# Performance work log

Measured on AMD Instinct MI355X. Metric: run time of the kernel, lower is better.

## Reference

```python
import jax, jax.numpy as jnp
import numpy as np

V, D, H, M, E, K = 32000, 1024, 1024, 64, 8, 2
B, S = 2, 2048


def _w(k, shape):
    fan_in = shape[-2] if len(shape) > 1 else shape[-1]
    return (jax.random.normal(k, shape, jnp.float32) / np.sqrt(fan_in)).astype(jnp.float32)


def setup_inputs() -> dict:
    key = jax.random.key(0)
    ks = jax.random.split(key, 24)
    HE = H // 2  # expert hidden = 512
    return {
        "input_ids": jax.random.randint(ks[0], (B, S), 0, V, dtype=jnp.int64),
        "emb": _w(ks[1], (V, D)),
        "enc_W": _w(ks[2], (D, H)), "enc_b": jnp.zeros((H,), jnp.float32),
        "s2c_W": _w(ks[3], (H, M)), "s2c_b": jnp.zeros((M,), jnp.float32),
        "rW1": _w(ks[4], (M, 64)), "rb1": jnp.zeros((64,), jnp.float32),
        "rW2": _w(ks[5], (64, E)), "rb2": jnp.zeros((E,), jnp.float32),
        "eW1": _w(ks[6], (E, M, HE)), "eb1": jnp.zeros((E, HE), jnp.float32),
        "eW2": _w(ks[7], (E, HE, M)), "eb2": jnp.zeros((E, M), jnp.float32),
        "c2s_W": _w(ks[8], (M, H)), "c2s_b": jnp.zeros((H,), jnp.float32),
        "dec_W": _w(ks[9], (H, D)), "dec_b": jnp.zeros((D,), jnp.float32),
        "out_W": _w(ks[10], (D, V)), "out_b": jnp.zeros((V,), jnp.float32),
    }


def reference(input_ids, emb, enc_W, enc_b, s2c_W, s2c_b, rW1, rb1, rW2, rb2,
              eW1, eb1, eW2, eb2, c2s_W, c2s_b, dec_W, dec_b, out_W, out_b):
    b, s = input_ids.shape
    n = b * s
    num_e = rW2.shape[1]
    # 1) embed + GIF encoder (linear + sigmoid spike-rate surrogate)
    x = emb[input_ids]                                   # (B,S,D)
    spikes_enc = jax.nn.sigmoid(x @ enc_W + enc_b)       # (B,S,H)
    # 2) spike -> continuous (rate coding over time window, then linear)
    cont = spikes_enc.reshape(n, -1) @ s2c_W + s2c_b     # (N,M)
    # 3) liquid MoE router: tanh MLP gate, softmax, top-k, renormalize
    gate_h = jnp.tanh(cont @ rW1 + rb1)
    probs = jax.nn.softmax(gate_h @ rW2 + rb2, axis=-1)  # (N,E)
    topv, topi = jax.lax.top_k(probs, K)                 # (N,K)
    wts = topv / jnp.sum(topv, axis=-1, keepdims=True)
    # per-token dense combine weights (zero for unselected experts) — matches
    # the original mask-and-sum over the full expert loop
    w_full = jnp.zeros((n, num_e), cont.dtype).at[jnp.arange(n)[:, None], topi].add(wts)
    # 4) all experts on all tokens (as in the source loop), then weighted combine
    h1 = jax.nn.relu(jnp.einsum('nm,emh->enh', cont, eW1) + eb1[:, None, :])  # (E,N,H/2)
    eo = jnp.einsum('enh,ehm->enm', h1, eW2) + eb2[:, None, :]                # (E,N,M)
    expert_out = jnp.einsum('ne,enm->nm', w_full, eo)                         # (N,M)
    # 5) continuous -> spike (Poisson expected rate) then time-average
    spikes_moe = jax.nn.sigmoid(expert_out @ c2s_W + c2s_b)                   # (N,H)
    spikes_avg = spikes_moe.reshape(b, s, -1)                                 # (B,S,H)
    # 6) GIF decoder + output projection
    decoded = jax.nn.sigmoid(spikes_avg @ dec_W + dec_b)                      # (B,S,D)
    logits = decoded @ out_W + out_b                                          # (B,S,V)
    return (logits, probs.reshape(b, s, num_e))
```

## Files before the change

kernel.cpp:

```cpp
#include <hip/hip_runtime.h>
#include <hip/hip_bf16.h>
#include <math.h>


typedef __bf16 bf16x8 __attribute__((ext_vector_type(8)));
typedef float f32x4 __attribute__((ext_vector_type(4)));

__device__ __forceinline__ ushort f2bf(float f) {
  union { float f; unsigned u; } v; v.f = f;
  unsigned u = v.u;
  u += 0x7FFFu + ((u >> 16) & 1u);
  return (ushort)(u >> 16);
}

__device__ __forceinline__ void async16(const void* g, void* l) {
  __builtin_amdgcn_global_load_lds((const __attribute__((address_space(1))) void*)g,
                                   (__attribute__((address_space(3))) void*)l,
                                   16, 0, 0);
}

__global__ void pack_w_kernel(const float* __restrict__ W, ushort* __restrict__ Wpk,
                              int K, int N) {
  long t = (long)blockIdx.x * blockDim.x + threadIdx.x;
  long total = (long)(K >> 3) * N;
  if (t >= total) return;
  long kb = t / N;
  int n = (int)(t - kb * N);
  long zoff = (long)blockIdx.y * K * N;
  const float* src = W + zoff + (kb * 8) * (long)N + n;
  union { ushort u[8]; uint4 v; } o;
#pragma unroll
  for (int j = 0; j < 8; ++j) o.u[j] = f2bf(src[(long)j * N]);
  *(uint4*)(Wpk + zoff + t * 8) = o.v;
}

__global__ void embed_pk_kernel(const int* __restrict__ ids, const float* __restrict__ emb,
                                ushort* __restrict__ xpk, int M) {
  int m = blockIdx.x * blockDim.x + threadIdx.x;
  int kb = blockIdx.y;
  long id = ids[m];
  const float4* s = (const float4*)(emb + id * 1024 + kb * 8);
  float4 a = s[0], b = s[1];
  union { ushort u[8]; uint4 v; } o;
  o.u[0] = f2bf(a.x); o.u[1] = f2bf(a.y); o.u[2] = f2bf(a.z); o.u[3] = f2bf(a.w);
  o.u[4] = f2bf(b.x); o.u[5] = f2bf(b.y); o.u[6] = f2bf(b.z); o.u[7] = f2bf(b.w);
  *(uint4*)(xpk + ((size_t)kb * M + m) * 8) = o.v;
}

template <int WAVES_M, int WAVES_N, int WM, int WN, int ACT, int OUT>
__launch_bounds__(WAVES_M * WAVES_N * 64)
__global__ void gemm_pk(const ushort* __restrict__ A, const ushort* __restrict__ B,
                        const float* __restrict__ bias, void* __restrict__ Cout,
                        int M, int N, int K, long sA, long sB, long sBias, long sC) {
  constexpr int BM = WAVES_M * WM * 16;
  constexpr int BN = WAVES_N * WN * 16;
  constexpr int NW = WAVES_M * WAVES_N;
  constexpr int ACH = 8 * BM / 64;
  constexpr int BCH = 8 * BN / 64;

  __shared__ ushort As[8 * BM * 8];
  __shared__ ushort Bs[8 * BN * 8];

  const int tid = threadIdx.x;
  const int lane = tid & 63;
  const int wave = tid >> 6;
  const int wm = wave % WAVES_M;
  const int wn = wave / WAVES_M;
  const int m0 = blockIdx.x * BM;
  const int n0 = blockIdx.y * BN;
  const int z = blockIdx.z;

  A += (size_t)z * sA;
  B += (size_t)z * sB;
  const float* biasp = bias + (size_t)z * sBias;

  f32x4 acc[WM][WN] = {};

  const int ktiles = K >> 6;
  const int q = lane >> 4;
  const int r16 = lane & 15;

  for (int kt = 0; kt < ktiles; ++kt) {
    const int kb0 = kt * 8;
#pragma unroll
    for (int c = wave; c < ACH; c += NW) {
      int kb = c / (BM / 64);
      int hh = c % (BM / 64);
      const ushort* g = A + (((size_t)(kb0 + kb)) * M + m0 + hh * 64 + lane) * 8;
      ushort* l = &As[(kb * BM + hh * 64) * 8];
      async16(g, l);
    }
#pragma unroll
    for (int c = wave; c < BCH; c += NW) {
      int kb = c / (BN / 64);
      int hh = c % (BN / 64);
      const ushort* g = B + (((size_t)(kb0 + kb)) * N + n0 + hh * 64 + lane) * 8;
      ushort* l = &Bs[(kb * BN + hh * 64) * 8];
      async16(g, l);
    }
    __syncthreads();
#pragma unroll
    for (int kk = 0; kk < 2; ++kk) {
      bf16x8 a[WM], b[WN];
#pragma unroll
      for (int mt = 0; mt < WM; ++mt)
        a[mt] = *(const bf16x8*)&As[((kk * 4 + q) * BM + wm * WM * 16 + mt * 16 + r16) * 8];
#pragma unroll
      for (int nt = 0; nt < WN; ++nt)
        b[nt] = *(const bf16x8*)&Bs[((kk * 4 + q) * BN + wn * WN * 16 + nt * 16 + r16) * 8];
#pragma unroll
      for (int mt = 0; mt < WM; ++mt)
#pragma unroll
        for (int nt = 0; nt < WN; ++nt)
          acc[mt][nt] = __builtin_amdgcn_mfma_f32_16x16x32_bf16(a[mt], b[nt], acc[mt][nt], 0, 0, 0);
    }
    __syncthreads();
  }

#pragma unroll
  for (int mt = 0; mt < WM; ++mt) {
#pragma unroll
    for (int nt = 0; nt < WN; ++nt) {
      int col = n0 + wn * WN * 16 + nt * 16 + r16;
      float bv = biasp[col];
#pragma unroll
      for (int r = 0; r < 4; ++r) {
        int row = m0 + wm * WM * 16 + mt * 16 + q * 4 + r;
        float v = acc[mt][nt][r] + bv;
        if (ACT == 1) v = 1.f / (1.f + expf(-v));
        else if (ACT == 2) v = fmaxf(v, 0.f);
        if (OUT == 0) {
          ((float*)Cout)[(size_t)z * sC + (size_t)row * N + col] = v;
        } else {
          ((ushort*)Cout)[(size_t)z * sC + ((size_t)(col >> 3) * M + row) * 8 + (col & 7)] = f2bf(v);
        }
      }
    }
  }
}

__global__ void s2c_kernel(const float* __restrict__ spikes, const float* __restrict__ W,
                           const float* __restrict__ b, float* __restrict__ cont,
                           ushort* __restrict__ contpk, int M) {
  int tid = threadIdx.x;
  int m = tid & 63;
  int n = blockIdx.x * 4 + (tid >> 6);
  const float* srow = spikes + (size_t)n * 1024;
  float acc = b[m];
#pragma unroll 8
  for (int k = 0; k < 1024; ++k) acc = fmaf(srow[k], W[k * 64 + m], acc);
  cont[(size_t)n * 64 + m] = acc;
  contpk[((size_t)(m >> 3) * M + n) * 8 + (m & 7)] = f2bf(acc);
}

__global__ void router_kernel(const float* __restrict__ cont, const float* __restrict__ rW1,
                              const float* __restrict__ rb1, const float* __restrict__ rW2,
                              const float* __restrict__ rb2, float* __restrict__ probs,
                              float* __restrict__ wfull) {
  int n = blockIdx.x;
  int L = threadIdx.x;
  float c = cont[(size_t)n * 64 + L];
  float gh = rb1[L];
#pragma unroll 8
  for (int k = 0; k < 64; ++k) {
    float ck = __shfl(c, k, 64);
    gh = fmaf(ck, rW1[k * 64 + L], gh);
  }
  gh = tanhf(gh);
  __shared__ float ghs[64];
  ghs[L] = gh;
  __syncthreads();
  float lg = 0.f;
  if (L < 8) {
    lg = rb2[L];
#pragma unroll 8
    for (int h = 0; h < 64; ++h) lg = fmaf(ghs[h], rW2[h * 8 + L], lg);
  }
  float mx = lg;
  for (int o = 4; o >= 1; o >>= 1) mx = fmaxf(mx, __shfl_xor(mx, o, 8));
  float ex = expf(lg - mx);
  float sm = ex;
  for (int o = 4; o >= 1; o >>= 1) sm += __shfl_xor(sm, o, 8);
  float pr = ex / sm;
  __shared__ float ps[8];
  if (L < 8) { probs[(size_t)n * 8 + L] = pr; ps[L] = pr; }
  __syncthreads();
  if (L == 0) {
    int i1 = 0; float v1 = ps[0];
#pragma unroll
    for (int e = 1; e < 8; ++e) if (ps[e] > v1) { v1 = ps[e]; i1 = e; }
    float v2 = -1.f; int i2 = 0;
#pragma unroll
    for (int e = 0; e < 8; ++e) if (e != i1 && ps[e] > v2) { v2 = ps[e]; i2 = e; }
    float s = v1 + v2;
    float w[8];
#pragma unroll
    for (int e = 0; e < 8; ++e) w[e] = 0.f;
    w[i1] = v1 / s; w[i2] = v2 / s;
#pragma unroll
    for (int e = 0; e < 8; ++e) wfull[(size_t)n * 8 + e] = w[e];
  }
}

__global__ void combine_kernel(const float* __restrict__ eo, const float* __restrict__ wfull,
                               ushort* __restrict__ exopk, int M) {
  int t = blockIdx.x * 256 + threadIdx.x;
  int n = t >> 6, m = t & 63;
  float acc = 0.f;
#pragma unroll
  for (int e = 0; e < 8; ++e)
    acc = fmaf(wfull[(size_t)n * 8 + e], eo[((size_t)e * M + n) * 64 + m], acc);
  exopk[((size_t)(m >> 3) * M + n) * 8 + (m & 7)] = f2bf(acc);
}

extern "C" void kernel_launch(void* const* d_in, const int* in_sizes, int n_in,
                              void* d_out, int out_size, void* d_ws, size_t ws_size,
                              hipStream_t stream) {
  const int*   ids   = (const int*)  d_in[0];
  const float* emb   = (const float*)d_in[1];
  const float* enc_W = (const float*)d_in[2];
  const float* enc_b = (const float*)d_in[3];
  const float* s2c_W = (const float*)d_in[4];
  const float* s2c_b = (const float*)d_in[5];
  const float* rW1   = (const float*)d_in[6];
  const float* rb1   = (const float*)d_in[7];
  const float* rW2   = (const float*)d_in[8];
  const float* rb2   = (const float*)d_in[9];
  const float* eW1   = (const float*)d_in[10];
  const float* eb1   = (const float*)d_in[11];
  const float* eW2   = (const float*)d_in[12];
  const float* eb2   = (const float*)d_in[13];
  const float* c2s_W = (const float*)d_in[14];
  const float* c2s_b = (const float*)d_in[15];
  const float* dec_W = (const float*)d_in[16];
  const float* dec_b = (const float*)d_in[17];
  const float* out_W = (const float*)d_in[18];
  const float* out_b = (const float*)d_in[19];
  (void)in_sizes; (void)n_in; (void)out_size; (void)ws_size;

  const int M = 4096, D = 1024, H = 1024, Mm = 64, E = 8, V = 32000, HE = 512;

  char* p = (char*)d_ws;
  auto alloc = [&](size_t bytes) { void* r = (void*)p; p += (bytes + 255) & ~(size_t)255; return r; };
  ushort* xpk    = (ushort*)alloc((size_t)M * D * 2);
  ushort* encWpk = (ushort*)alloc((size_t)D * H * 2);
  float*  spikes = (float*) alloc((size_t)M * H * 4);
  float*  cont   = (float*) alloc((size_t)M * Mm * 4);
  ushort* contpk = (ushort*)alloc((size_t)M * Mm * 2);
  float*  wfull  = (float*) alloc((size_t)M * E * 4);
  ushort* eW1pk  = (ushort*)alloc((size_t)E * Mm * HE * 2);
  ushort* eW2pk  = (ushort*)alloc((size_t)E * HE * Mm * 2);
  ushort* h1pk   = (ushort*)alloc((size_t)E * M * HE * 2);
  float*  eo     = (float*) alloc((size_t)E * M * Mm * 4);
  ushort* exopk  = (ushort*)alloc((size_t)M * Mm * 2);
  ushort* c2sWpk = (ushort*)alloc((size_t)Mm * H * 2);
  ushort* smoepk = (ushort*)alloc((size_t)M * H * 2);
  ushort* decWpk = (ushort*)alloc((size_t)H * D * 2);
  ushort* decpk  = (ushort*)alloc((size_t)M * D * 2);
  ushort* outWpk = (ushort*)alloc((size_t)D * V * 2);

  float* logits = (float*)d_out;
  float* probs  = logits + (size_t)M * V;

  pack_w_kernel<<<dim3(((D / 8) * H + 255) / 256, 1), 256, 0, stream>>>(enc_W, encWpk, D, H);
  pack_w_kernel<<<dim3(((Mm / 8) * HE + 255) / 256, E), 256, 0, stream>>>(eW1, eW1pk, Mm, HE);
  pack_w_kernel<<<dim3(((HE / 8) * Mm + 255) / 256, E), 256, 0, stream>>>(eW2, eW2pk, HE, Mm);
  pack_w_kernel<<<dim3(((Mm / 8) * H + 255) / 256, 1), 256, 0, stream>>>(c2s_W, c2sWpk, Mm, H);
  pack_w_kernel<<<dim3(((H / 8) * D + 255) / 256, 1), 256, 0, stream>>>(dec_W, decWpk, H, D);
  pack_w_kernel<<<dim3(((D / 8) * V + 255) / 256, 1), 256, 0, stream>>>(out_W, outWpk, D, V);

  embed_pk_kernel<<<dim3(M / 256, D / 8), 256, 0, stream>>>(ids, emb, xpk, M);
  gemm_pk<2, 2, 4, 4, 1, 0><<<dim3(M / 128, H / 128, 1), 256, 0, stream>>>(
      xpk, encWpk, enc_b, spikes, M, H, D, 0, 0, 0, 0);
  s2c_kernel<<<dim3(M / 4), 256, 0, stream>>>(spikes, s2c_W, s2c_b, cont, contpk, M);
  router_kernel<<<dim3(M), 64, 0, stream>>>(cont, rW1, rb1, rW2, rb2, probs, wfull);
  gemm_pk<2, 2, 4, 4, 2, 1><<<dim3(M / 128, HE / 128, E), 256, 0, stream>>>(
      contpk, eW1pk, eb1, h1pk, M, HE, Mm, 0, (long)Mm * HE, HE, (long)M * HE);
  gemm_pk<4, 1, 2, 4, 0, 0><<<dim3(M / 128, 1, E), 256, 0, stream>>>(
      h1pk, eW2pk, eb2, eo, M, Mm, HE, (long)M * HE, (long)HE * Mm, Mm, (long)M * Mm);
  combine_kernel<<<dim3(M * Mm / 256), 256, 0, stream>>>(eo, wfull, exopk, M);
  gemm_pk<2, 2, 4, 4, 1, 1><<<dim3(M / 128, H / 128, 1), 256, 0, stream>>>(
      exopk, c2sWpk, c2s_b, smoepk, M, H, Mm, 0, 0, 0, 0);
  gemm_pk<2, 2, 4, 4, 1, 1><<<dim3(M / 128, D / 128, 1), 256, 0, stream>>>(
      smoepk, decWpk, dec_b, decpk, M, D, H, 0, 0, 0, 0);
  gemm_pk<2, 2, 4, 4, 0, 0><<<dim3(M / 128, V / 128, 1), 256, 0, stream>>>(
      decpk, outWpk, out_b, logits, M, V, D, 0, 0, 0, 0);
}
```

Before: 1.124 ms.

## Add 256x256 eight-wave pipelined GEMM for the vocabulary output projection

```diff
diff --git a/kernel.cpp b/kernel.cpp
--- a/kernel.cpp
+++ b/kernel.cpp
@@ -135,6 +135,115 @@
           ((ushort*)Cout)[(size_t)z * sC + ((size_t)(col >> 3) * M + row) * 8 + (col & 7)] = f2bf(v);
         }
       }
+    }
+  }
+}
+
+
+#define PHASE(QQ, STAGE_STMT, WAIT_STMT)                                              \
+  {                                                                                   \
+    bf16x8 a[2][2];                                                                   \
+    _Pragma("unroll") for (int mi = 0; mi < 2; ++mi)                                  \
+      _Pragma("unroll") for (int kk = 0; kk < 2; ++kk)                                \
+        a[mi][kk] = *(const bf16x8*)&Ab[((kk * 4 + q) * 256 + wm * 128 +              \
+                                         ((QQ) * 2 + mi) * 16 + r16) * 8];            \
+    STAGE_STMT;                                                                       \
+    __builtin_amdgcn_s_barrier();                                                     \
+    asm volatile("s_waitcnt lgkmcnt(0)" ::: "memory");                                \
+    __builtin_amdgcn_sched_barrier(0);                                                \
+    __builtin_amdgcn_s_setprio(1);                                                    \
+    _Pragma("unroll") for (int kk = 0; kk < 2; ++kk)                                  \
+      _Pragma("unroll") for (int mi = 0; mi < 2; ++mi)                                \
+        _Pragma("unroll") for (int nf = 0; nf < 4; ++nf)                              \
+          acc[(QQ) * 2 + mi][nf] = __builtin_amdgcn_mfma_f32_16x16x32_bf16(           \
+              a[mi][kk], b[nf][kk], acc[(QQ) * 2 + mi][nf], 0, 0, 0);                 \
+    __builtin_amdgcn_s_setprio(0);                                                    \
+    __builtin_amdgcn_sched_barrier(0);                                                \
+    WAIT_STMT;                                                                        \
+    __builtin_amdgcn_s_barrier();                                                     \
+  }
+
+__global__ __launch_bounds__(512, 2)
+void gemm_out_8ph(const ushort* __restrict__ A, const ushort* __restrict__ B,
+                  const float* __restrict__ bias, float* __restrict__ C,
+                  int M, int N, int K) {
+  extern __shared__ ushort lds[];
+  const int tid = threadIdx.x;
+  const int lane = tid & 63;
+  const int wave = tid >> 6;
+  const int wm = wave & 1;
+  const int wn = wave >> 1;
+  const int q = lane >> 4;
+  const int r16 = lane & 15;
+
+  const int cpx = gridDim.x >> 3;
+  const int swz = ((int)blockIdx.x & 7) * cpx + ((int)blockIdx.x >> 3);
+  const int mtiles = M >> 8;
+  const int m0 = (swz % mtiles) << 8;
+  const int n0 = (swz / mtiles) << 8;
+
+  const int ktiles = K >> 6;
+
+  const int s_kb = wave >> 1;
+  const int s_row = ((wave & 1) << 6) + lane;
+
+  f32x4 acc[8][4] = {};
+
+  auto stageA = [&](int kt, int h) {
+    const int c = kt & 1;
+    size_t gk = (size_t)(kt * 8 + s_kb) * M + m0 + h * 128 + s_row;
+    ushort* l = lds + c * 32768 + (s_kb * 256 + h * 128 + s_row) * 8;
+    async16(A + gk * 8, l);
+    async16(A + (gk + (size_t)4 * M) * 8, l + 4 * 256 * 8);
+  };
+  auto stageB = [&](int kt, int h) {
+    const int c = kt & 1;
+    size_t gk = (size_t)(kt * 8 + s_kb) * N + n0 + h * 128 + s_row;
+    ushort* l = lds + c * 32768 + 16384 + (s_kb * 256 + h * 128 + s_row) * 8;
+    async16(B + gk * 8, l);
+    async16(B + (gk + (size_t)4 * N) * 8, l + 4 * 256 * 8);
+  };
+
+  stageB(0, 0); stageB(0, 1); stageA(0, 0); stageA(0, 1);
+  if (ktiles > 1) {
+    stageB(1, 0); stageB(1, 1);
+    asm volatile("s_waitcnt vmcnt(4)" ::: "memory");
+  } else {
+    asm volatile("s_waitcnt vmcnt(0)" ::: "memory");
+  }
+  __builtin_amdgcn_s_barrier();
+
+  for (int kt = 0; kt < ktiles; ++kt) {
+    __builtin_amdgcn_sched_barrier(0);
+    const ushort* Ab = lds + (kt & 1) * 32768;
+    const ushort* Bb = Ab + 16384;
+
+    bf16x8 b[4][2];
+#pragma unroll
+    for (int nf = 0; nf < 4; ++nf)
+#pragma unroll
+      for (int kk = 0; kk < 2; ++kk)
+        b[nf][kk] = *(const bf16x8*)&Bb[((kk * 4 + q) * 256 + wn * 64 + nf * 16 + r16) * 8];
+
+    PHASE(0, if (kt + 1 < ktiles) stageA(kt + 1, 0), (void)0)
+    PHASE(1, if (kt + 1 < ktiles) stageA(kt + 1, 1), (void)0)
+    PHASE(2, if (kt + 2 < ktiles) stageB(kt + 2, 0), (void)0)
+    PHASE(3, if (kt + 2 < ktiles) stageB(kt + 2, 1),
+          if (kt + 2 < ktiles) asm volatile("s_waitcnt vmcnt(4)" ::: "memory");
+          else asm volatile("s_waitcnt vmcnt(0)" ::: "memory"))
+  }
+
+#pragma unroll
+  for (int nf = 0; nf < 4; ++nf) {
+    const int col = n0 + wn * 64 + nf * 16 + r16;
+    const float bv = bias[col];
+#pragma unroll
+    for (int mf = 0; mf < 8; ++mf) {
+      const int row = m0 + wm * 128 + mf * 16 + q * 4;
+      float* out = C + (size_t)row * N + col;
+#pragma unroll
+      for (int r = 0; r < 4; ++r)
+        out[(size_t)r * N] = acc[mf][nf][r] + bv;
     }
   }
 }
@@ -262,6 +371,13 @@
   float* logits = (float*)d_out;
   float* probs  = logits + (size_t)M * V;
 
+  static bool attr_done = false;
+  if (!attr_done) {
+    (void)hipFuncSetAttribute(reinterpret_cast<const void*>(gemm_out_8ph),
+                              hipFuncAttributeMaxDynamicSharedMemorySize, 131072);
+    attr_done = true;
+  }
+
   pack_w_kernel<<<dim3(((D / 8) * H + 255) / 256, 1), 256, 0, stream>>>(enc_W, encWpk, D, H);
   pack_w_kernel<<<dim3(((Mm / 8) * HE + 255) / 256, E), 256, 0, stream>>>(eW1, eW1pk, Mm, HE);
   pack_w_kernel<<<dim3(((HE / 8) * Mm + 255) / 256, E), 256, 0, stream>>>(eW2, eW2pk, HE, Mm);
@@ -283,6 +399,6 @@
       exopk, c2sWpk, c2s_b, smoepk, M, H, Mm, 0, 0, 0, 0);
   gemm_pk<2, 2, 4, 4, 1, 1><<<dim3(M / 128, D / 128, 1), 256, 0, stream>>>(
       smoepk, decWpk, dec_b, decpk, M, D, H, 0, 0, 0, 0);
-  gemm_pk<2, 2, 4, 4, 0, 0><<<dim3(M / 128, V / 128, 1), 256, 0, stream>>>(
-      decpk, outWpk, out_b, logits, M, V, D, 0, 0, 0, 0);
-}
+  gemm_out_8ph<<<dim3((M / 256) * (V / 256)), 512, 131072, stream>>>(
+      decpk, outWpk, out_b, logits, M, V, D);
+}
```

Measured after the change: 1.159 ms. 1.03x slower.

## Add pipelined 256x256 MFMA kernel for the output vocabulary projection

Applied to the files above, without the earlier changes.

```diff
diff --git a/kernel.cpp b/kernel.cpp
--- a/kernel.cpp
+++ b/kernel.cpp
@@ -135,6 +135,150 @@
           ((ushort*)Cout)[(size_t)z * sC + ((size_t)(col >> 3) * M + row) * 8 + (col & 7)] = f2bf(v);
         }
       }
+    }
+  }
+}
+
+
+#define SBAR0 __builtin_amdgcn_sched_barrier(0)
+#define FULLBAR { SBAR0; __builtin_amdgcn_s_barrier(); SBAR0; }
+
+#define CH_PLAIN(STAGE_STMT, LD_STMT, MF_STMT)  \
+  {                                             \
+    STAGE_STMT;                                 \
+    LD_STMT;                                    \
+    SBAR0;                                      \
+    __builtin_amdgcn_s_setprio(1);              \
+    MF_STMT;                                    \
+    __builtin_amdgcn_s_setprio(0);              \
+    FULLBAR;                                    \
+  }
+
+#define CH_GATE(STAGE_STMT, VMC, LD_STMT, MF_STMT)          \
+  {                                                         \
+    STAGE_STMT;                                             \
+    asm volatile("s_waitcnt vmcnt(" #VMC ")" ::: "memory"); \
+    FULLBAR;                                                \
+    LD_STMT;                                                \
+    SBAR0;                                                  \
+    __builtin_amdgcn_s_setprio(1);                          \
+    MF_STMT;                                                \
+    __builtin_amdgcn_s_setprio(0);                          \
+    FULLBAR;                                                \
+  }
+
+template <int Mc, int Nc, int Kc>
+__global__ __launch_bounds__(512, 2)
+void gemm_out_pipe(const ushort* __restrict__ A, const ushort* __restrict__ B,
+                   const float* __restrict__ bias, float* __restrict__ C) {
+  static_assert((Kc / 64) >= 4 && (Kc / 64) % 2 == 0, "need even ktiles >= 4");
+  extern __shared__ ushort lds[];
+  const int tid = threadIdx.x;
+  const int lane = tid & 63;
+  const int wave = tid >> 6;
+  const int wm = wave & 1;
+  const int wn = wave >> 1;
+  const int q = lane >> 4;
+  const int r16 = lane & 15;
+
+  const int cpx = gridDim.x >> 3;
+  const int swz = ((int)blockIdx.x & 7) * cpx + ((int)blockIdx.x >> 3);
+  constexpr int mtiles = Mc >> 8;
+  const int m0 = (swz % mtiles) << 8;
+  const int n0 = (swz / mtiles) << 8;
+
+  const int s_kb = wave >> 1;
+  const int s_row = ((wave & 1) << 6) + lane;
+
+  f32x4 acc[8][4] = {};
+  bf16x8 aE[2][2], aO[2][2], bA[4][2], bB[4][2];
+
+  auto stageA = [&](int kt, int h) {
+    size_t gk = ((size_t)(kt * 8 + s_kb) * Mc + m0 + h * 128 + s_row) * 8;
+    ushort* l = lds + (size_t)(kt & 1) * 32768 + (s_kb * 256 + h * 128 + s_row) * 8;
+    async16(A + gk, l);
+    async16(A + gk + (size_t)4 * Mc * 8, l + 4 * 256 * 8);
+  };
+  auto stageB = [&](int kt, int h) {
+    size_t gk = ((size_t)(kt * 8 + s_kb) * Nc + n0 + h * 128 + s_row) * 8;
+    ushort* l = lds + (size_t)(kt & 1) * 32768 + 16384 + (s_kb * 256 + h * 128 + s_row) * 8;
+    async16(B + gk, l);
+    async16(B + gk + (size_t)4 * Nc * 8, l + 4 * 256 * 8);
+  };
+  auto LDA = [&](int buf, int QQ, bf16x8 (&a)[2][2]) {
+#pragma unroll
+    for (int mi = 0; mi < 2; ++mi)
+#pragma unroll
+      for (int kk = 0; kk < 2; ++kk)
+        a[mi][kk] = *(const bf16x8*)&lds[(size_t)buf * 32768 +
+                                         ((kk * 4 + q) * 256 + wm * 128 + (QQ * 2 + mi) * 16 + r16) * 8];
+  };
+  auto LDB = [&](int buf, bf16x8 (&b)[4][2]) {
+#pragma unroll
+    for (int nf = 0; nf < 4; ++nf)
+#pragma unroll
+      for (int kk = 0; kk < 2; ++kk)
+        b[nf][kk] = *(const bf16x8*)&lds[(size_t)buf * 32768 + 16384 +
+                                         ((kk * 4 + q) * 256 + wn * 64 + nf * 16 + r16) * 8];
+  };
+  auto MF = [&](int QQ, bf16x8 (&a)[2][2], bf16x8 (&b)[4][2]) {
+#pragma unroll
+    for (int kk = 0; kk < 2; ++kk)
+#pragma unroll
+      for (int mi = 0; mi < 2; ++mi)
+#pragma unroll
+        for (int nf = 0; nf < 4; ++nf)
+          acc[QQ * 2 + mi][nf] =
+              __builtin_amdgcn_mfma_f32_16x16x32_bf16(a[mi][kk], b[nf][kk], acc[QQ * 2 + mi][nf], 0, 0, 0);
+  };
+
+  constexpr int ktiles = Kc >> 6;
+
+  stageB(0, 0); stageB(0, 1);
+  stageA(0, 0); stageA(0, 1);
+  stageB(1, 0); stageB(1, 1);
+  asm volatile("s_waitcnt vmcnt(4)" ::: "memory");
+  FULLBAR;
+  LDB(0, bA);
+  LDA(0, 0, aE);
+
+  for (int J = 0; J < ktiles / 2 - 1; ++J) {
+    const int t = 2 * J;
+    CH_PLAIN(stageA(t + 1, 0), LDA(0, 1, aO), MF(0, aE, bA));
+    CH_PLAIN(stageA(t + 1, 1), LDA(0, 2, aE), MF(1, aO, bA));
+    CH_PLAIN(stageB(t + 2, 0), LDA(0, 3, aO), MF(2, aE, bA));
+    CH_GATE (stageB(t + 2, 1), 4, { LDB(1, bB); LDA(1, 0, aE); }, MF(3, aO, bA));
+    CH_PLAIN(stageA(t + 2, 0), LDA(1, 1, aO), MF(0, aE, bB));
+    CH_PLAIN(stageA(t + 2, 1), LDA(1, 2, aE), MF(1, aO, bB));
+    CH_PLAIN(stageB(t + 3, 0), LDA(1, 3, aO), MF(2, aE, bB));
+    CH_GATE (stageB(t + 3, 1), 4, { LDB(0, bA); LDA(0, 0, aE); }, MF(3, aO, bB));
+  }
+
+  {
+    const int t = ktiles - 2;
+    CH_PLAIN(stageA(t + 1, 0), LDA(0, 1, aO), MF(0, aE, bA));
+    CH_PLAIN(stageA(t + 1, 1), LDA(0, 2, aE), MF(1, aO, bA));
+    CH_PLAIN((void)0,          LDA(0, 3, aO), MF(2, aE, bA));
+    CH_GATE ((void)0, 0, { LDB(1, bB); LDA(1, 0, aE); }, MF(3, aO, bA));
+    CH_PLAIN((void)0, LDA(1, 1, aO), MF(0, aE, bB));
+    CH_PLAIN((void)0, LDA(1, 2, aE), MF(1, aO, bB));
+    CH_PLAIN((void)0, LDA(1, 3, aO), MF(2, aE, bB));
+    __builtin_amdgcn_s_setprio(1);
+    MF(3, aO, bB);
+    __builtin_amdgcn_s_setprio(0);
+  }
+
+#pragma unroll
+  for (int nf = 0; nf < 4; ++nf) {
+    const int col = n0 + wn * 64 + nf * 16 + r16;
+    const float bv = bias[col];
+#pragma unroll
+    for (int mf = 0; mf < 8; ++mf) {
+      const int row = m0 + wm * 128 + mf * 16 + q * 4;
+      float* out = C + (size_t)row * Nc + col;
+#pragma unroll
+      for (int r = 0; r < 4; ++r)
+        __builtin_nontemporal_store(acc[mf][nf][r] + bv, out + (size_t)r * Nc);
     }
   }
 }
@@ -262,6 +406,13 @@
   float* logits = (float*)d_out;
   float* probs  = logits + (size_t)M * V;
 
+  static bool attr_done = false;
+  if (!attr_done) {
+    (void)hipFuncSetAttribute(reinterpret_cast<const void*>(&gemm_out_pipe<4096, 32000, 1024>),
+                              hipFuncAttributeMaxDynamicSharedMemorySize, 131072);
+    attr_done = true;
+  }
+
   pack_w_kernel<<<dim3(((D / 8) * H + 255) / 256, 1), 256, 0, stream>>>(enc_W, encWpk, D, H);
   pack_w_kernel<<<dim3(((Mm / 8) * HE + 255) / 256, E), 256, 0, stream>>>(eW1, eW1pk, Mm, HE);
   pack_w_kernel<<<dim3(((HE / 8) * Mm + 255) / 256, E), 256, 0, stream>>>(eW2, eW2pk, HE, Mm);
@@ -283,6 +434,6 @@
       exopk, c2sWpk, c2s_b, smoepk, M, H, Mm, 0, 0, 0, 0);
   gemm_pk<2, 2, 4, 4, 1, 1><<<dim3(M / 128, D / 128, 1), 256, 0, stream>>>(
       smoepk, decWpk, dec_b, decpk, M, D, H, 0, 0, 0, 0);
-  gemm_pk<2, 2, 4, 4, 0, 0><<<dim3(M / 128, V / 128, 1), 256, 0, stream>>>(
-      decpk, outWpk, out_b, logits, M, V, D, 0, 0, 0, 0);
-}
+  gemm_out_pipe<4096, 32000, 1024><<<dim3((M / 256) * (V / 256)), 512, 131072, stream>>>(
+      decpk, outWpk, out_b, logits);
+}
```

After: 1.630 ms. 45.0% more time.
